# Optimization experiments

Hardware: AMD Instinct MI355X
Metric: run time of the kernel (lower is better)

The kernel has to match this reference:

```python
import jax, jax.numpy as jnp
import numpy as np

NUM_HEADS = 4
NUM_GROUPS = 32
EPS = 1e-5


def group_norm(x, gamma, beta):
    B, C, H, W = x.shape
    g = x.reshape(B, NUM_GROUPS, C // NUM_GROUPS, H, W)
    mean = g.mean(axis=(2, 3, 4), keepdims=True)
    var = g.var(axis=(2, 3, 4), keepdims=True)
    g = (g - mean) * jax.lax.rsqrt(var + EPS)
    x = g.reshape(B, C, H, W)
    return x * gamma[None, :, None, None] + beta[None, :, None, None]


def setup_inputs() -> dict:
    key = jax.random.key(0)
    ks = jax.random.split(key, 7)
    B, C, H, W = 16, 256, 32, 32
    x = jax.random.normal(ks[0], (B, C, H, W), dtype=jnp.float32)
    gn_gamma = jnp.ones((C,), dtype=jnp.float32)
    gn_beta = jnp.zeros((C,), dtype=jnp.float32)
    s = 1.0 / np.sqrt(C)
    qkv_w = jax.random.normal(ks[1], (3 * C, C), dtype=jnp.float32) * s
    qkv_b = jnp.zeros((3 * C,), dtype=jnp.float32)
    proj_w = jax.random.normal(ks[2], (C, C), dtype=jnp.float32) * s
    proj_b = jnp.zeros((C,), dtype=jnp.float32)
    return {"x": x, "gn_gamma": gn_gamma, "gn_beta": gn_beta,
            "qkv_w": qkv_w, "qkv_b": qkv_b, "proj_w": proj_w, "proj_b": proj_b}


def reference(x, gn_gamma, gn_beta, qkv_w, qkv_b, proj_w, proj_b):
    B, C, H, W = x.shape
    nh = NUM_HEADS
    d = C // nh
    N = H * W

    h = group_norm(x, gn_gamma, gn_beta)
    # 1x1 conv == channel matmul
    qkv = jnp.einsum('bchw,oc->bohw', h, qkv_w) + qkv_b[None, :, None, None]
    qkv = qkv.reshape(B, 3, nh, d, N)
    q, k, v = qkv[:, 0], qkv[:, 1], qkv[:, 2]  # each [B, nh, d, N]

    scale = 1.0 / jnp.sqrt(jnp.asarray(d, dtype=x.dtype))
    attn = jnp.einsum('bhdn,bhdm->bhnm', q, k) * scale  # [B, nh, N, N]
    attn = jax.nn.softmax(attn, axis=-1)
    out = jnp.einsum('bhnm,bhdm->bhdn', attn, v)  # [B, nh, d, N]
    out = out.reshape(B, C, H, W)

    out = jnp.einsum('bchw,oc->bohw', out, proj_w) + proj_b[None, :, None, None]
    return x + out
```

## Files before the change

kernel.cpp:

```cpp
#include <hip/hip_runtime.h>
#include <math.h>

typedef unsigned short u16;
typedef unsigned int u32;
typedef __attribute__((ext_vector_type(8))) short s16x8;
typedef __attribute__((ext_vector_type(4))) float f32x4;

#define NB 16
#define NN 1024
#define GN_EPS 1e-5f

static __device__ __forceinline__ u16 f2bf(float f) {
    union { float f; u32 u; } v; v.f = f;
    return (u16)((v.u + 0x8000u) >> 16);
}
static __device__ __forceinline__ u32 pk2(float a, float b) {
    union { float f; u32 u; } A, B; A.f = a; B.f = b;
    return __builtin_amdgcn_perm(A.u + 0x8000u, B.u + 0x8000u, 0x03020706u);
}
static __device__ __forceinline__ u32 cvtpk2(float a, float b) {
    u32 r;
    asm("v_cvt_pk_bf16_f32 %0, %1, %2" : "=v"(r) : "v"(a), "v"(b));
    return r;
}

#define GLL16(gp, lp) __builtin_amdgcn_global_load_lds( \
    (const __attribute__((address_space(1))) void*)(const void*)(gp), \
    (__attribute__((address_space(3))) void*)(void*)(lp), 16, 0, 0)

__global__ __launch_bounds__(256) void gn_fused_kernel(
    const float* __restrict__ x, const float* __restrict__ gamma,
    const float* __restrict__ beta, u16* __restrict__ Xtg)
{
    const int gg = blockIdx.x;
    const int b  = blockIdx.y;
    const int t  = threadIdx.x;
    __shared__ float T[8 * 1028];
    __shared__ float red[8];
    __shared__ float sstat[2];

    const float4* xb = (const float4*)(x + ((size_t)b * 32 + gg) * 8192);
    float s = 0.f, ss = 0.f;
#pragma unroll
    for (int i = 0; i < 8; ++i) {
        float4 f = xb[i * 256 + t];
        *(float4*)&T[i * 1028 + t * 4] = f;
        s  += f.x + f.y + f.z + f.w;
        ss += f.x * f.x + f.y * f.y + f.z * f.z + f.w * f.w;
    }
#pragma unroll
    for (int off = 32; off > 0; off >>= 1) {
        s  += __shfl_down(s, off);
        ss += __shfl_down(ss, off);
    }
    if ((t & 63) == 0) { red[t >> 6] = s; red[4 + (t >> 6)] = ss; }
    __syncthreads();
    if (t == 0) {
        float sa = red[0] + red[1] + red[2] + red[3];
        float sb = red[4] + red[5] + red[6] + red[7];
        float mean = sa * (1.0f / 8192.0f);
        float var  = sb * (1.0f / 8192.0f) - mean * mean;
        sstat[0] = mean; sstat[1] = 1.0f / sqrtf(var + GN_EPS);
    }
    __syncthreads();
    const float mean = sstat[0], rstd = sstat[1];
    float gm[8], bt[8];
#pragma unroll
    for (int j = 0; j < 8; ++j) {
        float gj = gamma[gg * 8 + j];
        gm[j] = gj * rstd;
        bt[j] = beta[gg * 8 + j] - mean * rstd * gj;
    }
    u16* dst = Xtg + ((size_t)(b * 32 + gg) * NN) * 8;
#pragma unroll
    for (int rep = 0; rep < 4; ++rep) {
        int n = rep * 256 + t;
        u32 o[4];
#pragma unroll
        for (int p = 0; p < 4; ++p) {
            float v0 = T[(2 * p)     * 1028 + n] * gm[2 * p]     + bt[2 * p];
            float v1 = T[(2 * p + 1) * 1028 + n] * gm[2 * p + 1] + bt[2 * p + 1];
            o[p] = pk2(v0, v1);
        }
        *(uint4*)(dst + (size_t)n * 8) = make_uint4(o[0], o[1], o[2], o[3]);
    }
}

__global__ __launch_bounds__(256) void wcvt_kernel(
    const float* __restrict__ qkv_w, const float* __restrict__ proj_w,
    u16* __restrict__ wqb, u16* __restrict__ wpb)
{
    int i = blockIdx.x * 256 + threadIdx.x;
    if (i < 49152) {
        float4 f = ((const float4*)qkv_w)[i];
        *(uint2*)(wqb + (size_t)i * 4) = make_uint2(pk2(f.x, f.y), pk2(f.z, f.w));
    } else {
        int j = i - 49152;
        float4 f = ((const float4*)proj_w)[j];
        *(uint2*)(wpb + (size_t)j * 4) = make_uint2(pk2(f.x, f.y), pk2(f.z, f.w));
    }
}

__global__ __launch_bounds__(256, 4) void qkv_mfma_kernel(
    const u16* __restrict__ Wb, const float* __restrict__ bias,
    const u16* __restrict__ Xtg,
    u16* __restrict__ qh, u16* __restrict__ kh, u16* __restrict__ vh)
{
    const int b = blockIdx.z, ot = blockIdx.y, nt = blockIdx.x;
    const int t = threadIdx.x, w = t >> 6, l = t & 63;
    const int g = l >> 4, c = l & 15;
    __shared__ u16 Slds[32 * 512];
    const u16* Xb = Xtg + (size_t)b * 32 * NN * 8;

    if (ot < 4) {
        const int h = ot;
        const size_t bhoff = (size_t)(b * 4 + h) << 16;
        const u16* Wq = Wb + (size_t)(h)     * 64 * 256;
        const u16* Wk = Wb + (size_t)(4 + h) * 64 * 256;

#pragma unroll
        for (int s = w; s < 32; s += 4) {
            int osub = s >> 3, ks = s & 7;
            GLL16(Wq + (size_t)(osub * 16 + c) * 256 + ks * 32 + g * 8, Slds + s * 512);
        }
        s16x8 a0[8], a1[8];
#pragma unroll
        for (int ks = 0; ks < 8; ++ks) {
            a0[ks] = *(const s16x8*)(Xb + ((size_t)(ks * 4 + g) * NN + nt * 128 + (2 * w) * 16 + c) * 8);
            a1[ks] = *(const s16x8*)(Xb + ((size_t)(ks * 4 + g) * NN + nt * 128 + (2 * w + 1) * 16 + c) * 8);
        }
        f32x4 acc[2][4];
#pragma unroll
        for (int i = 0; i < 2; ++i)
#pragma unroll
            for (int j = 0; j < 4; ++j) acc[i][j] = (f32x4){0.f, 0.f, 0.f, 0.f};
        __syncthreads();
#pragma unroll
        for (int ks = 0; ks < 8; ++ks)
#pragma unroll
            for (int j = 0; j < 4; ++j) {
                s16x8 bf = *(const s16x8*)(Slds + (j * 8 + ks) * 512 + l * 8);
                acc[0][j] = __builtin_amdgcn_mfma_f32_16x16x32_bf16(a0[ks], bf, acc[0][j], 0, 0, 0);
                acc[1][j] = __builtin_amdgcn_mfma_f32_16x16x32_bf16(a1[ks], bf, acc[1][j], 0, 0, 0);
            }
        __syncthreads();

#pragma unroll
        for (int s = w; s < 32; s += 4) {
            int osub = s >> 3, ks = s & 7;
            GLL16(Wk + (size_t)(osub * 16 + c) * 256 + ks * 32 + g * 8, Slds + s * 512);
        }
        {
            const float sc = 0.125f * 1.44269504088896f;
            float bv[4];
#pragma unroll
            for (int j = 0; j < 4; ++j) bv[j] = bias[h * 64 + j * 16 + c];
            u16* dst = qh + bhoff + (size_t)(nt * 128) * 64;
#pragma unroll
            for (int i = 0; i < 2; ++i)
#pragma unroll
                for (int j = 0; j < 4; ++j)
#pragma unroll
                    for (int r = 0; r < 4; ++r) {
                        int n = (2 * w + i) * 16 + g * 4 + r;
                        dst[(size_t)n * 64 + j * 16 + c] = f2bf((acc[i][j][r] + bv[j]) * sc);
                    }
        }
#pragma unroll
        for (int i = 0; i < 2; ++i)
#pragma unroll
            for (int j = 0; j < 4; ++j) acc[i][j] = (f32x4){0.f, 0.f, 0.f, 0.f};
        asm volatile("s_waitcnt vmcnt(32)" ::: "memory");
        __builtin_amdgcn_s_barrier();
        asm volatile("" ::: "memory");
#pragma unroll
        for (int ks = 0; ks < 8; ++ks)
#pragma unroll
            for (int j = 0; j < 4; ++j) {
                s16x8 bf = *(const s16x8*)(Slds + (j * 8 + ks) * 512 + l * 8);
                acc[0][j] = __builtin_amdgcn_mfma_f32_16x16x32_bf16(a0[ks], bf, acc[0][j], 0, 0, 0);
                acc[1][j] = __builtin_amdgcn_mfma_f32_16x16x32_bf16(a1[ks], bf, acc[1][j], 0, 0, 0);
            }
        {
            float bv[4];
#pragma unroll
            for (int j = 0; j < 4; ++j) bv[j] = bias[(4 + h) * 64 + j * 16 + c];
            u16* dst = kh + bhoff + (size_t)(nt * 128) * 64;
#pragma unroll
            for (int i = 0; i < 2; ++i)
#pragma unroll
                for (int j = 0; j < 4; ++j)
#pragma unroll
                    for (int r = 0; r < 4; ++r) {
                        int n = (2 * w + i) * 16 + g * 4 + r;
                        dst[(size_t)n * 64 + j * 16 + c] = f2bf(acc[i][j][r] + bv[j]);
                    }
        }
    } else {
        const int h = ot - 4;
        const size_t bhoff = (size_t)(b * 4 + h) << 16;
        const u16* Wo = Wb + (size_t)(8 + h) * 64 * 256;
        f32x4 acc[8];
#pragma unroll
        for (int j = 0; j < 8; ++j) acc[j] = (f32x4){0.f, 0.f, 0.f, 0.f};
        for (int kk = 0; kk < 256; kk += 128) {
            if (kk) __syncthreads();
#pragma unroll
            for (int s = w; s < 32; s += 4) {
                int nsub = s >> 2, ks = s & 3;
                GLL16(Xb + ((size_t)((kk >> 3) + ks * 4 + g) * NN + nt * 128 + nsub * 16 + c) * 8, Slds + s * 512);
            }
            __syncthreads();
#pragma unroll
            for (int ks = 0; ks < 4; ++ks) {
                s16x8 a = *(const s16x8*)(Wo + (size_t)(w * 16 + c) * 256 + kk + ks * 32 + g * 8);
#pragma unroll
                for (int j = 0; j < 8; ++j) {
                    s16x8 xf = *(const s16x8*)(Slds + (j * 4 + ks) * 512 + l * 8);
                    acc[j] = __builtin_amdgcn_mfma_f32_16x16x32_bf16(a, xf, acc[j], 0, 0, 0);
                }
            }
        }
        float bv[4];
#pragma unroll
        for (int r = 0; r < 4; ++r) bv[r] = bias[(8 + h) * 64 + w * 16 + g * 4 + r];
        u16* dst = vh + bhoff;
#pragma unroll
        for (int j = 0; j < 8; ++j)
#pragma unroll
            for (int r = 0; r < 4; ++r) {
                int d = w * 16 + g * 4 + r;
                int m = nt * 128 + j * 16 + c;
                dst[(size_t)d * NN + m] = f2bf(acc[j][r] + bv[r]);
            }
    }
}

__global__ __launch_bounds__(512, 4) void attn_mfma_kernel(
    const u16* __restrict__ qh, const u16* __restrict__ kh,
    const u16* __restrict__ vh, u16* __restrict__ aoT)
{
    const int t = threadIdx.x;
    const int w = t >> 6, l = t & 63;
    const int g = l >> 4, c = l & 15;
    const int bid = blockIdx.x;
    const int xcd = bid & 7;
    const int idx = bid >> 3;
    const int qt  = idx & 7;
    const int grp = (idx >> 3) * 8 + xcd;
    const int b = grp >> 2, h = grp & 3;
    const size_t bhoff = (size_t)grp << 16;
    const int n_base = qt * 128 + w * 16;

    __shared__ u16 Klds[4][8 * 512];
    __shared__ u16 Vlds[4][8 * 512];
    __shared__ u16 Plds[8][2 * 512];

    const u16* qb = qh + bhoff;
    const u16* kb = kh + bhoff;
    const u16* vb = vh + bhoff;

    const int msub = w >> 1, uu = w & 1;

    s16x8 qf[2];
#pragma unroll
    for (int u = 0; u < 2; ++u)
        qf[u] = *(const s16x8*)(qb + (size_t)(n_base + c) * 64 + u * 32 + g * 8);

    s16x8 onef;
#pragma unroll
    for (int j = 0; j < 8; ++j) onef[j] = (short)0x3F80;

    f32x4 Oacc[4];
    f32x4 Lacc = (f32x4){0.f, 0.f, 0.f, 0.f};
#pragma unroll
    for (int ds = 0; ds < 4; ++ds) Oacc[ds] = (f32x4){0.f, 0.f, 0.f, 0.f};

    u16* pw = &Plds[w][0];

#define STK(tt) GLL16(kb + (size_t)((tt) * 64 + msub * 16 + c) * 64 + uu * 32 + g * 8, &Klds[(tt) & 3][w * 512])
#define STV(tt) GLL16(vb + (size_t)(msub * 16 + c) * NN + (tt) * 64 + uu * 32 + g * 8, &Vlds[(tt) & 3][w * 512])

    auto tile = [&](int buf) {
        const u16* Kc = &Klds[buf][0];
        const u16* Vc = &Vlds[buf][0];
        f32x4 S[4];
#pragma unroll
        for (int ms = 0; ms < 4; ++ms) S[ms] = (f32x4){0.f, 0.f, 0.f, 0.f};
        __builtin_amdgcn_s_setprio(1);
#pragma unroll
        for (int ms = 0; ms < 4; ++ms)
#pragma unroll
            for (int u = 0; u < 2; ++u) {
                s16x8 af = *(const s16x8*)(Kc + (ms * 2 + u) * 512 + l * 8);
                S[ms] = __builtin_amdgcn_mfma_f32_16x16x32_bf16(af, qf[u], S[ms], 0, 0, 0);
            }
        __builtin_amdgcn_s_setprio(0);
        s16x8 vf[4][2];
#pragma unroll
        for (int ds = 0; ds < 4; ++ds)
#pragma unroll
            for (int u = 0; u < 2; ++u)
                vf[ds][u] = *(const s16x8*)(Vc + (ds * 2 + u) * 512 + l * 8);
#pragma unroll
        for (int ms = 0; ms < 4; ++ms)
#pragma unroll
            for (int r = 0; r < 4; ++r) S[ms][r] = __builtin_amdgcn_exp2f(S[ms][r]);
#pragma unroll
        for (int ms = 0; ms < 4; ++ms) {
            u32 d0 = cvtpk2(S[ms][0], S[ms][1]);
            u32 d1 = cvtpk2(S[ms][2], S[ms][3]);
            int off = (ms >> 1) * 512 + ((ms & 1) * 2 + (g >> 1)) * 128 + c * 8 + (g & 1) * 4;
            *(uint2*)(pw + off) = make_uint2(d0, d1);
        }
        __builtin_amdgcn_s_setprio(1);
#pragma unroll
        for (int u = 0; u < 2; ++u) {
            s16x8 pf = *(const s16x8*)(pw + u * 512 + l * 8);
#pragma unroll
            for (int ds = 0; ds < 4; ++ds)
                Oacc[ds] = __builtin_amdgcn_mfma_f32_16x16x32_bf16(vf[ds][u], pf, Oacc[ds], 0, 0, 0);
            Lacc = __builtin_amdgcn_mfma_f32_16x16x32_bf16(onef, pf, Lacc, 0, 0, 0);
        }
        __builtin_amdgcn_s_setprio(0);
    };

    STK(0); STV(0); STK(1); STV(1);

    for (int it = 0; it < 8; ++it) {
        if (it < 7) {
            STK(2 * it + 2); STV(2 * it + 2);
            STK(2 * it + 3); STV(2 * it + 3);
            asm volatile("s_waitcnt vmcnt(4)" ::: "memory");
        } else {
            asm volatile("s_waitcnt vmcnt(0)" ::: "memory");
        }
        __builtin_amdgcn_s_barrier();
        asm volatile("" ::: "memory");

        tile((2 * it) & 3);
        tile((2 * it + 1) & 3);

        asm volatile("" ::: "memory");
        __builtin_amdgcn_s_barrier();
    }

    u16* aob = aoT + (size_t)b * NN * 256 + h * 64;
    float inv = 1.0f / Lacc[0];
    const size_t nrow = (size_t)(n_base + c) * 256;
#pragma unroll
    for (int ds = 0; ds < 4; ++ds) {
        u32 lo = cvtpk2(Oacc[ds][0] * inv, Oacc[ds][1] * inv);
        u32 hi = cvtpk2(Oacc[ds][2] * inv, Oacc[ds][3] * inv);
        *(uint2*)(aob + nrow + ds * 16 + g * 4) = make_uint2(lo, hi);
    }
#undef STK
#undef STV
}

__global__ __launch_bounds__(256) void proj_mfma_kernel(
    const u16* __restrict__ Wb, const float* __restrict__ bias,
    const u16* __restrict__ aoT, const float* __restrict__ x,
    float* __restrict__ out)
{
    const int b = blockIdx.z, ot = blockIdx.y, nt = blockIdx.x;
    const int t = threadIdx.x, w = t >> 6, l = t & 63;
    const int g = l >> 4, c = l & 15;
    __shared__ u16 Slds[32 * 512];
    const u16* Xb = aoT + ((size_t)b * NN + nt * 128) * 256;
    const u16* Wo = Wb + (size_t)ot * 64 * 256;

    f32x4 acc[8];
#pragma unroll
    for (int j = 0; j < 8; ++j) acc[j] = (f32x4){0.f, 0.f, 0.f, 0.f};
    for (int kk = 0; kk < 256; kk += 128) {
        if (kk) __syncthreads();
#pragma unroll
        for (int s = w; s < 32; s += 4) {
            int nsub = s >> 2, ks = s & 3;
            GLL16(Xb + (size_t)(nsub * 16 + c) * 256 + kk + ks * 32 + g * 8, Slds + s * 512);
        }
        __syncthreads();
#pragma unroll
        for (int ks = 0; ks < 4; ++ks) {
            s16x8 a = *(const s16x8*)(Wo + (size_t)(w * 16 + c) * 256 + kk + ks * 32 + g * 8);
#pragma unroll
            for (int j = 0; j < 8; ++j) {
                s16x8 xf = *(const s16x8*)(Slds + (j * 4 + ks) * 512 + l * 8);
                acc[j] = __builtin_amdgcn_mfma_f32_16x16x32_bf16(a, xf, acc[j], 0, 0, 0);
            }
        }
    }
    float bv[4];
#pragma unroll
    for (int r = 0; r < 4; ++r) bv[r] = bias[ot * 64 + w * 16 + g * 4 + r];
#pragma unroll
    for (int j = 0; j < 8; ++j)
#pragma unroll
        for (int r = 0; r < 4; ++r) {
            int o = ot * 64 + w * 16 + g * 4 + r;
            int n = nt * 128 + j * 16 + c;
            size_t addr = ((size_t)b * 256 + o) * NN + n;
            out[addr] = acc[j][r] + bv[r] + x[addr];
        }
}

extern "C" void kernel_launch(void* const* d_in, const int* in_sizes, int n_in,
                              void* d_out, int out_size, void* d_ws, size_t ws_size,
                              hipStream_t stream)
{
    const float* x      = (const float*)d_in[0];
    const float* gamma  = (const float*)d_in[1];
    const float* beta   = (const float*)d_in[2];
    const float* qkv_w  = (const float*)d_in[3];
    const float* qkv_b  = (const float*)d_in[4];
    const float* proj_w = (const float*)d_in[5];
    const float* proj_b = (const float*)d_in[6];
    float* out = (float*)d_out;

    float* ws = (float*)d_ws;
    u16* Xtg = (u16*)(ws + 1024);
    u16* wqb = Xtg + (size_t)4194304;
    u16* wpb = wqb + (size_t)196608;
    u16* qh  = wpb + (size_t)65536;
    u16* kh  = qh + (size_t)4194304;
    u16* vh  = kh + (size_t)4194304;
    u16* aoT = vh + (size_t)4194304;

    wcvt_kernel<<<dim3(256), 256, 0, stream>>>(qkv_w, proj_w, wqb, wpb);
    gn_fused_kernel<<<dim3(32, NB), 256, 0, stream>>>(x, gamma, beta, Xtg);

    qkv_mfma_kernel<<<dim3(8, 8, NB), 256, 0, stream>>>(
        wqb, qkv_b, Xtg, qh, kh, vh);

    attn_mfma_kernel<<<dim3(512), 512, 0, stream>>>(qh, kh, vh, aoT);

    proj_mfma_kernel<<<dim3(8, 4, NB), 256, 0, stream>>>(
        wpb, proj_b, aoT, x, out);
}
```

Baseline: 74.10 us.

## Process two query sub-tiles per wave in attention, halving block threads

The attention kernel now runs 4 waves per block instead of 8. Each wave handles 32 query rows as two 16-row sub-tiles and reuses every K and V fragment it reads from LDS across both sub-tiles. Each wave also issues twice as many global-to-LDS loads per stage, and the wait counts are adjusted to match. The intent is to cut LDS read traffic per MFMA and raise MFMA density, at the cost of more registers per wave and fewer waves to hide latency.

```diff
diff --git a/kernel.cpp b/kernel.cpp
--- a/kernel.cpp
+++ b/kernel.cpp
@@ -236,7 +236,7 @@
     }
 }
 
-__global__ __launch_bounds__(512, 4) void attn_mfma_kernel(
+__global__ __launch_bounds__(256, 2) void attn_mfma_kernel(
     const u16* __restrict__ qh, const u16* __restrict__ kh,
     const u16* __restrict__ vh, u16* __restrict__ aoT)
 {
@@ -250,50 +250,58 @@
     const int grp = (idx >> 3) * 8 + xcd;
     const int b = grp >> 2, h = grp & 3;
     const size_t bhoff = (size_t)grp << 16;
-    const int n_base = qt * 128 + w * 16;
+    const int n_base = qt * 128 + w * 32;
 
     __shared__ u16 Klds[4][8 * 512];
     __shared__ u16 Vlds[4][8 * 512];
-    __shared__ u16 Plds[8][2 * 512];
+    __shared__ u16 Plds[4][4 * 512];
 
     const u16* qb = qh + bhoff;
     const u16* kb = kh + bhoff;
     const u16* vb = vh + bhoff;
 
-    const int msub = w >> 1, uu = w & 1;
-
-    s16x8 qf[2];
-#pragma unroll
-    for (int u = 0; u < 2; ++u)
-        qf[u] = *(const s16x8*)(qb + (size_t)(n_base + c) * 64 + u * 32 + g * 8);
+    s16x8 qf[2][2];
+#pragma unroll
+    for (int sub = 0; sub < 2; ++sub)
+#pragma unroll
+        for (int u = 0; u < 2; ++u)
+            qf[sub][u] = *(const s16x8*)(qb + (size_t)(n_base + sub * 16 + c) * 64 + u * 32 + g * 8);
 
     s16x8 onef;
 #pragma unroll
     for (int j = 0; j < 8; ++j) onef[j] = (short)0x3F80;
 
-    f32x4 Oacc[4];
-    f32x4 Lacc = (f32x4){0.f, 0.f, 0.f, 0.f};
-#pragma unroll
-    for (int ds = 0; ds < 4; ++ds) Oacc[ds] = (f32x4){0.f, 0.f, 0.f, 0.f};
+    f32x4 Oacc[2][4];
+    f32x4 Lacc[2];
+#pragma unroll
+    for (int sub = 0; sub < 2; ++sub) {
+        Lacc[sub] = (f32x4){0.f, 0.f, 0.f, 0.f};
+#pragma unroll
+        for (int ds = 0; ds < 4; ++ds) Oacc[sub][ds] = (f32x4){0.f, 0.f, 0.f, 0.f};
+    }
 
     u16* pw = &Plds[w][0];
 
-#define STK(tt) GLL16(kb + (size_t)((tt) * 64 + msub * 16 + c) * 64 + uu * 32 + g * 8, &Klds[(tt) & 3][w * 512])
-#define STV(tt) GLL16(vb + (size_t)(msub * 16 + c) * NN + (tt) * 64 + uu * 32 + g * 8, &Vlds[(tt) & 3][w * 512])
+#define STK(tt, s) GLL16(kb + (size_t)((tt) * 64 + ((s) >> 1) * 16 + c) * 64 + ((s) & 1) * 32 + g * 8, &Klds[(tt) & 3][(s) * 512])
+#define STV(tt, s) GLL16(vb + (size_t)(((s) >> 1) * 16 + c) * NN + (tt) * 64 + ((s) & 1) * 32 + g * 8, &Vlds[(tt) & 3][(s) * 512])
+#define STAGE(tt) do { STK(tt, w); STK(tt, w + 4); STV(tt, w); STV(tt, w + 4); } while (0)
 
     auto tile = [&](int buf) {
         const u16* Kc = &Klds[buf][0];
         const u16* Vc = &Vlds[buf][0];
-        f32x4 S[4];
-#pragma unroll
-        for (int ms = 0; ms < 4; ++ms) S[ms] = (f32x4){0.f, 0.f, 0.f, 0.f};
+        f32x4 S[2][4];
+#pragma unroll
+        for (int sub = 0; sub < 2; ++sub)
+#pragma unroll
+            for (int ms = 0; ms < 4; ++ms) S[sub][ms] = (f32x4){0.f, 0.f, 0.f, 0.f};
         __builtin_amdgcn_s_setprio(1);
 #pragma unroll
         for (int ms = 0; ms < 4; ++ms)
 #pragma unroll
             for (int u = 0; u < 2; ++u) {
                 s16x8 af = *(const s16x8*)(Kc + (ms * 2 + u) * 512 + l * 8);
-                S[ms] = __builtin_amdgcn_mfma_f32_16x16x32_bf16(af, qf[u], S[ms], 0, 0, 0);
+                S[0][ms] = __builtin_amdgcn_mfma_f32_16x16x32_bf16(af, qf[0][u], S[0][ms], 0, 0, 0);
+                S[1][ms] = __builtin_amdgcn_mfma_f32_16x16x32_bf16(af, qf[1][u], S[1][ms], 0, 0, 0);
             }
         __builtin_amdgcn_s_setprio(0);
         s16x8 vf[4][2];
@@ -303,35 +311,41 @@
             for (int u = 0; u < 2; ++u)
                 vf[ds][u] = *(const s16x8*)(Vc + (ds * 2 + u) * 512 + l * 8);
 #pragma unroll
-        for (int ms = 0; ms < 4; ++ms)
-#pragma unroll
-            for (int r = 0; r < 4; ++r) S[ms][r] = __builtin_amdgcn_exp2f(S[ms][r]);
-#pragma unroll
-        for (int ms = 0; ms < 4; ++ms) {
-            u32 d0 = cvtpk2(S[ms][0], S[ms][1]);
-            u32 d1 = cvtpk2(S[ms][2], S[ms][3]);
-            int off = (ms >> 1) * 512 + ((ms & 1) * 2 + (g >> 1)) * 128 + c * 8 + (g & 1) * 4;
-            *(uint2*)(pw + off) = make_uint2(d0, d1);
-        }
+        for (int sub = 0; sub < 2; ++sub)
+#pragma unroll
+            for (int ms = 0; ms < 4; ++ms)
+#pragma unroll
+                for (int r = 0; r < 4; ++r) S[sub][ms][r] = __builtin_amdgcn_exp2f(S[sub][ms][r]);
+#pragma unroll
+        for (int sub = 0; sub < 2; ++sub)
+#pragma unroll
+            for (int ms = 0; ms < 4; ++ms) {
+                u32 d0 = cvtpk2(S[sub][ms][0], S[sub][ms][1]);
+                u32 d1 = cvtpk2(S[sub][ms][2], S[sub][ms][3]);
+                int off = (sub * 2 + (ms >> 1)) * 512 + ((ms & 1) * 2 + (g >> 1)) * 128 + c * 8 + (g & 1) * 4;
+                *(uint2*)(pw + off) = make_uint2(d0, d1);
+            }
         __builtin_amdgcn_s_setprio(1);
 #pragma unroll
-        for (int u = 0; u < 2; ++u) {
-            s16x8 pf = *(const s16x8*)(pw + u * 512 + l * 8);
-#pragma unroll
-            for (int ds = 0; ds < 4; ++ds)
-                Oacc[ds] = __builtin_amdgcn_mfma_f32_16x16x32_bf16(vf[ds][u], pf, Oacc[ds], 0, 0, 0);
-            Lacc = __builtin_amdgcn_mfma_f32_16x16x32_bf16(onef, pf, Lacc, 0, 0, 0);
-        }
+        for (int sub = 0; sub < 2; ++sub)
+#pragma unroll
+            for (int u = 0; u < 2; ++u) {
+                s16x8 pf = *(const s16x8*)(pw + (sub * 2 + u) * 512 + l * 8);
+#pragma unroll
+                for (int ds = 0; ds < 4; ++ds)
+                    Oacc[sub][ds] = __builtin_amdgcn_mfma_f32_16x16x32_bf16(vf[ds][u], pf, Oacc[sub][ds], 0, 0, 0);
+                Lacc[sub] = __builtin_amdgcn_mfma_f32_16x16x32_bf16(onef, pf, Lacc[sub], 0, 0, 0);
+            }
         __builtin_amdgcn_s_setprio(0);
     };
 
-    STK(0); STV(0); STK(1); STV(1);
+    STAGE(0); STAGE(1);
 
     for (int it = 0; it < 8; ++it) {
         if (it < 7) {
-            STK(2 * it + 2); STV(2 * it + 2);
-            STK(2 * it + 3); STV(2 * it + 3);
-            asm volatile("s_waitcnt vmcnt(4)" ::: "memory");
+            STAGE(2 * it + 2);
+            STAGE(2 * it + 3);
+            asm volatile("s_waitcnt vmcnt(8)" ::: "memory");
         } else {
             asm volatile("s_waitcnt vmcnt(0)" ::: "memory");
         }
@@ -346,16 +360,20 @@
     }
 
     u16* aob = aoT + (size_t)b * NN * 256 + h * 64;
-    float inv = 1.0f / Lacc[0];
-    const size_t nrow = (size_t)(n_base + c) * 256;
-#pragma unroll
-    for (int ds = 0; ds < 4; ++ds) {
-        u32 lo = cvtpk2(Oacc[ds][0] * inv, Oacc[ds][1] * inv);
-        u32 hi = cvtpk2(Oacc[ds][2] * inv, Oacc[ds][3] * inv);
-        *(uint2*)(aob + nrow + ds * 16 + g * 4) = make_uint2(lo, hi);
+#pragma unroll
+    for (int sub = 0; sub < 2; ++sub) {
+        float inv = 1.0f / Lacc[sub][0];
+        const size_t nrow = (size_t)(n_base + sub * 16 + c) * 256;
+#pragma unroll
+        for (int ds = 0; ds < 4; ++ds) {
+            u32 lo = cvtpk2(Oacc[sub][ds][0] * inv, Oacc[sub][ds][1] * inv);
+            u32 hi = cvtpk2(Oacc[sub][ds][2] * inv, Oacc[sub][ds][3] * inv);
+            *(uint2*)(aob + nrow + ds * 16 + g * 4) = make_uint2(lo, hi);
+        }
     }
 #undef STK
 #undef STV
+#undef STAGE
 }
 
 __global__ __launch_bounds__(256) void proj_mfma_kernel(
@@ -433,7 +451,7 @@
     qkv_mfma_kernel<<<dim3(8, 8, NB), 256, 0, stream>>>(
         wqb, qkv_b, Xtg, qh, kh, vh);
 
-    attn_mfma_kernel<<<dim3(512), 512, 0, stream>>>(qh, kh, vh, aoT);
+    attn_mfma_kernel<<<dim3(512), 256, 0, stream>>>(qh, kh, vh, aoT);
 
     proj_mfma_kernel<<<dim3(8, 4, NB), 256, 0, stream>>>(
         wpb, proj_b, aoT, x, out);
```

Result: no change. 74.44 us (+0.5%).

## Fuse V projection into Q/K blocks to reuse register-held X tiles

Applied to the files above, without the earlier changes.

The QKV projection kernel previously launched separate blocks for Q/K and for V, each reloading the normalized input tile. Now each block computes Q, K, then V for one head, reusing the X fragments already held in registers and streaming the V weights through LDS with the same double-use pattern, swapping MFMA operand order to produce V in transposed layout. This halves the grid and removes the duplicate X reads, at the cost of longer per-block serial work, fewer blocks for latency hiding, and a dropped occupancy hint in launch bounds.

```diff
diff --git a/kernel.cpp b/kernel.cpp
--- a/kernel.cpp
+++ b/kernel.cpp
@@ -101,137 +101,138 @@
     }
 }
 
-__global__ __launch_bounds__(256, 4) void qkv_mfma_kernel(
+__global__ __launch_bounds__(256) void qkv_mfma_kernel(
     const u16* __restrict__ Wb, const float* __restrict__ bias,
     const u16* __restrict__ Xtg,
     u16* __restrict__ qh, u16* __restrict__ kh, u16* __restrict__ vh)
 {
-    const int b = blockIdx.z, ot = blockIdx.y, nt = blockIdx.x;
+    const int b = blockIdx.z, h = blockIdx.y, nt = blockIdx.x;
     const int t = threadIdx.x, w = t >> 6, l = t & 63;
     const int g = l >> 4, c = l & 15;
     __shared__ u16 Slds[32 * 512];
     const u16* Xb = Xtg + (size_t)b * 32 * NN * 8;
-
-    if (ot < 4) {
-        const int h = ot;
-        const size_t bhoff = (size_t)(b * 4 + h) << 16;
-        const u16* Wq = Wb + (size_t)(h)     * 64 * 256;
-        const u16* Wk = Wb + (size_t)(4 + h) * 64 * 256;
-
-#pragma unroll
-        for (int s = w; s < 32; s += 4) {
-            int osub = s >> 3, ks = s & 7;
-            GLL16(Wq + (size_t)(osub * 16 + c) * 256 + ks * 32 + g * 8, Slds + s * 512);
-        }
-        s16x8 a0[8], a1[8];
-#pragma unroll
-        for (int ks = 0; ks < 8; ++ks) {
-            a0[ks] = *(const s16x8*)(Xb + ((size_t)(ks * 4 + g) * NN + nt * 128 + (2 * w) * 16 + c) * 8);
-            a1[ks] = *(const s16x8*)(Xb + ((size_t)(ks * 4 + g) * NN + nt * 128 + (2 * w + 1) * 16 + c) * 8);
-        }
-        f32x4 acc[2][4];
+    const size_t bhoff = (size_t)(b * 4 + h) << 16;
+    const u16* Wq = Wb + (size_t)(h)     * 64 * 256;
+    const u16* Wk = Wb + (size_t)(4 + h) * 64 * 256;
+    const u16* Wv = Wb + (size_t)(8 + h) * 64 * 256;
+
+#pragma unroll
+    for (int s = w; s < 32; s += 4) {
+        int osub = s >> 3, ks = s & 7;
+        GLL16(Wq + (size_t)(osub * 16 + c) * 256 + ks * 32 + g * 8, Slds + s * 512);
+    }
+    s16x8 a0[8], a1[8];
+#pragma unroll
+    for (int ks = 0; ks < 8; ++ks) {
+        a0[ks] = *(const s16x8*)(Xb + ((size_t)(ks * 4 + g) * NN + nt * 128 + (2 * w) * 16 + c) * 8);
+        a1[ks] = *(const s16x8*)(Xb + ((size_t)(ks * 4 + g) * NN + nt * 128 + (2 * w + 1) * 16 + c) * 8);
+    }
+    f32x4 acc[2][4];
+#pragma unroll
+    for (int i = 0; i < 2; ++i)
+#pragma unroll
+        for (int j = 0; j < 4; ++j) acc[i][j] = (f32x4){0.f, 0.f, 0.f, 0.f};
+    __syncthreads();
+
+#pragma unroll
+    for (int ks = 0; ks < 8; ++ks)
+#pragma unroll
+        for (int j = 0; j < 4; ++j) {
+            s16x8 bf = *(const s16x8*)(Slds + (j * 8 + ks) * 512 + l * 8);
+            acc[0][j] = __builtin_amdgcn_mfma_f32_16x16x32_bf16(a0[ks], bf, acc[0][j], 0, 0, 0);
+            acc[1][j] = __builtin_amdgcn_mfma_f32_16x16x32_bf16(a1[ks], bf, acc[1][j], 0, 0, 0);
+        }
+    __syncthreads();
+
+#pragma unroll
+    for (int s = w; s < 32; s += 4) {
+        int osub = s >> 3, ks = s & 7;
+        GLL16(Wk + (size_t)(osub * 16 + c) * 256 + ks * 32 + g * 8, Slds + s * 512);
+    }
+    {
+        const float sc = 0.125f * 1.44269504088896f;
+        float bv[4];
+#pragma unroll
+        for (int j = 0; j < 4; ++j) bv[j] = bias[h * 64 + j * 16 + c];
+        u16* dst = qh + bhoff + (size_t)(nt * 128) * 64;
 #pragma unroll
         for (int i = 0; i < 2; ++i)
 #pragma unroll
-            for (int j = 0; j < 4; ++j) acc[i][j] = (f32x4){0.f, 0.f, 0.f, 0.f};
-        __syncthreads();
-#pragma unroll
-        for (int ks = 0; ks < 8; ++ks)
-#pragma unroll
-            for (int j = 0; j < 4; ++j) {
-                s16x8 bf = *(const s16x8*)(Slds + (j * 8 + ks) * 512 + l * 8);
-                acc[0][j] = __builtin_amdgcn_mfma_f32_16x16x32_bf16(a0[ks], bf, acc[0][j], 0, 0, 0);
-                acc[1][j] = __builtin_amdgcn_mfma_f32_16x16x32_bf16(a1[ks], bf, acc[1][j], 0, 0, 0);
-            }
-        __syncthreads();
-
-#pragma unroll
-        for (int s = w; s < 32; s += 4) {
-            int osub = s >> 3, ks = s & 7;
-            GLL16(Wk + (size_t)(osub * 16 + c) * 256 + ks * 32 + g * 8, Slds + s * 512);
-        }
-        {
-            const float sc = 0.125f * 1.44269504088896f;
-            float bv[4];
-#pragma unroll
-            for (int j = 0; j < 4; ++j) bv[j] = bias[h * 64 + j * 16 + c];
-            u16* dst = qh + bhoff + (size_t)(nt * 128) * 64;
-#pragma unroll
-            for (int i = 0; i < 2; ++i)
-#pragma unroll
-                for (int j = 0; j < 4; ++j)
-#pragma unroll
-                    for (int r = 0; r < 4; ++r) {
-                        int n = (2 * w + i) * 16 + g * 4 + r;
-                        dst[(size_t)n * 64 + j * 16 + c] = f2bf((acc[i][j][r] + bv[j]) * sc);
-                    }
-        }
+            for (int j = 0; j < 4; ++j)
+#pragma unroll
+                for (int r = 0; r < 4; ++r) {
+                    int n = (2 * w + i) * 16 + g * 4 + r;
+                    dst[(size_t)n * 64 + j * 16 + c] = f2bf((acc[i][j][r] + bv[j]) * sc);
+                }
+    }
+#pragma unroll
+    for (int i = 0; i < 2; ++i)
+#pragma unroll
+        for (int j = 0; j < 4; ++j) acc[i][j] = (f32x4){0.f, 0.f, 0.f, 0.f};
+    asm volatile("s_waitcnt vmcnt(32)" ::: "memory");
+    __builtin_amdgcn_s_barrier();
+    asm volatile("" ::: "memory");
+
+#pragma unroll
+    for (int ks = 0; ks < 8; ++ks)
+#pragma unroll
+        for (int j = 0; j < 4; ++j) {
+            s16x8 bf = *(const s16x8*)(Slds + (j * 8 + ks) * 512 + l * 8);
+            acc[0][j] = __builtin_amdgcn_mfma_f32_16x16x32_bf16(a0[ks], bf, acc[0][j], 0, 0, 0);
+            acc[1][j] = __builtin_amdgcn_mfma_f32_16x16x32_bf16(a1[ks], bf, acc[1][j], 0, 0, 0);
+        }
+    __syncthreads();
+
+#pragma unroll
+    for (int s = w; s < 32; s += 4) {
+        int osub = s >> 3, ks = s & 7;
+        GLL16(Wv + (size_t)(osub * 16 + c) * 256 + ks * 32 + g * 8, Slds + s * 512);
+    }
+    {
+        float bv[4];
+#pragma unroll
+        for (int j = 0; j < 4; ++j) bv[j] = bias[(4 + h) * 64 + j * 16 + c];
+        u16* dst = kh + bhoff + (size_t)(nt * 128) * 64;
 #pragma unroll
         for (int i = 0; i < 2; ++i)
 #pragma unroll
-            for (int j = 0; j < 4; ++j) acc[i][j] = (f32x4){0.f, 0.f, 0.f, 0.f};
-        asm volatile("s_waitcnt vmcnt(32)" ::: "memory");
-        __builtin_amdgcn_s_barrier();
-        asm volatile("" ::: "memory");
-#pragma unroll
-        for (int ks = 0; ks < 8; ++ks)
-#pragma unroll
-            for (int j = 0; j < 4; ++j) {
-                s16x8 bf = *(const s16x8*)(Slds + (j * 8 + ks) * 512 + l * 8);
-                acc[0][j] = __builtin_amdgcn_mfma_f32_16x16x32_bf16(a0[ks], bf, acc[0][j], 0, 0, 0);
-                acc[1][j] = __builtin_amdgcn_mfma_f32_16x16x32_bf16(a1[ks], bf, acc[1][j], 0, 0, 0);
-            }
-        {
-            float bv[4];
-#pragma unroll
-            for (int j = 0; j < 4; ++j) bv[j] = bias[(4 + h) * 64 + j * 16 + c];
-            u16* dst = kh + bhoff + (size_t)(nt * 128) * 64;
-#pragma unroll
-            for (int i = 0; i < 2; ++i)
-#pragma unroll
-                for (int j = 0; j < 4; ++j)
-#pragma unroll
-                    for (int r = 0; r < 4; ++r) {
-                        int n = (2 * w + i) * 16 + g * 4 + r;
-                        dst[(size_t)n * 64 + j * 16 + c] = f2bf(acc[i][j][r] + bv[j]);
-                    }
-        }
-    } else {
-        const int h = ot - 4;
-        const size_t bhoff = (size_t)(b * 4 + h) << 16;
-        const u16* Wo = Wb + (size_t)(8 + h) * 64 * 256;
-        f32x4 acc[8];
-#pragma unroll
-        for (int j = 0; j < 8; ++j) acc[j] = (f32x4){0.f, 0.f, 0.f, 0.f};
-        for (int kk = 0; kk < 256; kk += 128) {
-            if (kk) __syncthreads();
-#pragma unroll
-            for (int s = w; s < 32; s += 4) {
-                int nsub = s >> 2, ks = s & 3;
-                GLL16(Xb + ((size_t)((kk >> 3) + ks * 4 + g) * NN + nt * 128 + nsub * 16 + c) * 8, Slds + s * 512);
-            }
-            __syncthreads();
-#pragma unroll
-            for (int ks = 0; ks < 4; ++ks) {
-                s16x8 a = *(const s16x8*)(Wo + (size_t)(w * 16 + c) * 256 + kk + ks * 32 + g * 8);
-#pragma unroll
-                for (int j = 0; j < 8; ++j) {
-                    s16x8 xf = *(const s16x8*)(Slds + (j * 4 + ks) * 512 + l * 8);
-                    acc[j] = __builtin_amdgcn_mfma_f32_16x16x32_bf16(a, xf, acc[j], 0, 0, 0);
+            for (int j = 0; j < 4; ++j)
+#pragma unroll
+                for (int r = 0; r < 4; ++r) {
+                    int n = (2 * w + i) * 16 + g * 4 + r;
+                    dst[(size_t)n * 64 + j * 16 + c] = f2bf(acc[i][j][r] + bv[j]);
                 }
-            }
-        }
-        float bv[4];
-#pragma unroll
-        for (int r = 0; r < 4; ++r) bv[r] = bias[(8 + h) * 64 + w * 16 + g * 4 + r];
+    }
+    f32x4 vacc[4][2];
+#pragma unroll
+    for (int osub = 0; osub < 4; ++osub)
+#pragma unroll
+        for (int i = 0; i < 2; ++i) vacc[osub][i] = (f32x4){0.f, 0.f, 0.f, 0.f};
+    asm volatile("s_waitcnt vmcnt(32)" ::: "memory");
+    __builtin_amdgcn_s_barrier();
+    asm volatile("" ::: "memory");
+
+#pragma unroll
+    for (int ks = 0; ks < 8; ++ks)
+#pragma unroll
+        for (int osub = 0; osub < 4; ++osub) {
+            s16x8 wf = *(const s16x8*)(Slds + (osub * 8 + ks) * 512 + l * 8);
+            vacc[osub][0] = __builtin_amdgcn_mfma_f32_16x16x32_bf16(wf, a0[ks], vacc[osub][0], 0, 0, 0);
+            vacc[osub][1] = __builtin_amdgcn_mfma_f32_16x16x32_bf16(wf, a1[ks], vacc[osub][1], 0, 0, 0);
+        }
+    {
         u16* dst = vh + bhoff;
 #pragma unroll
-        for (int j = 0; j < 8; ++j)
+        for (int osub = 0; osub < 4; ++osub)
 #pragma unroll
             for (int r = 0; r < 4; ++r) {
-                int d = w * 16 + g * 4 + r;
-                int m = nt * 128 + j * 16 + c;
-                dst[(size_t)d * NN + m] = f2bf(acc[j][r] + bv[r]);
+                int d = osub * 16 + g * 4 + r;
+                float bi = bias[(8 + h) * 64 + d];
+#pragma unroll
+                for (int i = 0; i < 2; ++i) {
+                    int m = nt * 128 + (2 * w + i) * 16 + c;
+                    dst[(size_t)d * NN + m] = f2bf(vacc[osub][i][r] + bi);
+                }
             }
     }
 }
@@ -430,7 +431,7 @@
     wcvt_kernel<<<dim3(256), 256, 0, stream>>>(qkv_w, proj_w, wqb, wpb);
     gn_fused_kernel<<<dim3(32, NB), 256, 0, stream>>>(x, gamma, beta, Xtg);
 
-    qkv_mfma_kernel<<<dim3(8, 8, NB), 256, 0, stream>>>(
+    qkv_mfma_kernel<<<dim3(8, 4, NB), 256, 0, stream>>>(
         wqb, qkv_b, Xtg, qh, kh, vh);
 
     attn_mfma_kernel<<<dim3(512), 512, 0, stream>>>(qh, kh, vh, aoT);
```

After: 71.97 us (median of 2 runs). 2.9% less time.
